# Optimization experiments

Hardware: AMD Instinct MI355X
Metric: run time of the kernel (lower is better)

The kernel has to match this reference:

```python
import jax, jax.numpy as jnp
import numpy as np

UNITS = 300
MDN_MIXES = 8  # Config.mdn_mixes: 3*8=24 MDN params + 1 length = 25-dim feedback
FEAT = 25
GATE_IN = 2 * FEAT  # concat(inputs, prev_output)


def setup_inputs() -> dict:
    key = jax.random.key(0)
    ks = jax.random.split(key, 12)
    B, T = 2048, 512
    x = jax.random.uniform(ks[0], (B, T, FEAT), dtype=jnp.float32)
    s = 0.05
    kernel = jax.random.normal(ks[1], (FEAT, 4 * UNITS), dtype=jnp.float32) * s
    recurrent_kernel = jax.random.normal(ks[2], (UNITS, 4 * UNITS), dtype=jnp.float32) * s
    # unit_forget_bias: zeros except forget-gate slice = ones
    bias = jnp.concatenate([
        jnp.zeros((UNITS,), jnp.float32),
        jnp.ones((UNITS,), jnp.float32),
        jnp.zeros((2 * UNITS,), jnp.float32),
    ])
    # MLPGate: 2-layer MLP combining the two 25-dim distributions -> 24-dim
    mlp_w1 = jax.random.normal(ks[3], (GATE_IN, GATE_IN), dtype=jnp.float32) * s
    mlp_b1 = jnp.zeros((GATE_IN,), jnp.float32)
    mlp_w2 = jax.random.normal(ks[4], (GATE_IN, FEAT - 1), dtype=jnp.float32) * s
    mlp_b2 = jnp.zeros((FEAT - 1,), jnp.float32)
    # MDN heads on h (units -> mdn_mixes each)
    wa = jax.random.normal(ks[5], (UNITS, MDN_MIXES), dtype=jnp.float32) * s
    ba = jnp.zeros((MDN_MIXES,), jnp.float32)
    wm = jax.random.normal(ks[6], (UNITS, MDN_MIXES), dtype=jnp.float32) * s
    bm = jnp.zeros((MDN_MIXES,), jnp.float32)
    ws = jax.random.normal(ks[7], (UNITS, MDN_MIXES), dtype=jnp.float32) * s
    bs = jnp.zeros((MDN_MIXES,), jnp.float32)
    return {
        'x': x, 'kernel': kernel, 'recurrent_kernel': recurrent_kernel, 'bias': bias,
        'mlp_w1': mlp_w1, 'mlp_b1': mlp_b1, 'mlp_w2': mlp_w2, 'mlp_b2': mlp_b2,
        'wa': wa, 'ba': ba, 'wm': wm, 'bm': bm, 'ws': ws, 'bs': bs,
    }


def _hard_sigmoid(z):
    return jnp.clip(0.2 * z + 0.5, 0.0, 1.0)


def _nnelu(z):
    return 1.0 + jax.nn.elu(z)


def reference(x, kernel, recurrent_kernel, bias,
              mlp_w1, mlp_b1, mlp_w2, mlp_b2,
              wa, ba, wm, bm, ws, bs):
    B = x.shape[0]
    dt = x.dtype

    def step(carry, xt):
        h, c, prev = carry  # [B,U], [B,U], [B,25]
        il = xt[:, 24:25]
        pl = prev[:, 24:25]
        combined = il + pl
        denom = jnp.maximum(combined, jnp.asarray(1e-8, dt))  # LengthNormalizer
        inp2 = jnp.concatenate([xt[:, :24], il / denom], axis=1)
        prev2 = jnp.concatenate([prev[:, :24], pl / denom], axis=1)
        # MLP gate combining the two distributions
        g = jax.nn.relu(jnp.concatenate([inp2, prev2], axis=1) @ mlp_w1 + mlp_b1)
        g = g @ mlp_w2 + mlp_b2  # [B,24]
        gate_out = jnp.concatenate([g, combined], axis=1)  # [B,25]
        # LSTM gates (split-kernel math == fused without dropout)
        z = gate_out @ kernel + h @ recurrent_kernel + bias  # [B,4U]
        zi, zf, zc, zo = jnp.split(z, 4, axis=1)
        i = _hard_sigmoid(zi)
        f = _hard_sigmoid(zf)
        o = _hard_sigmoid(zo)
        c_new = f * c + i * jnp.tanh(zc)
        h_new = o * jnp.tanh(c_new)
        # MDN heads
        alpha = jax.nn.softmax(h_new @ wa + ba, axis=-1)
        mu = h_new @ wm + bm
        sigma = _nnelu(h_new @ ws + bs)
        mdn = jnp.concatenate([alpha, mu, sigma, combined], axis=1)  # [B,25]
        return (h_new, c_new, mdn), mdn

    h0 = jnp.zeros((B, UNITS), dt)
    c0 = jnp.zeros((B, UNITS), dt)
    prev0 = jnp.zeros((B, FEAT), dt)
    xt = jnp.swapaxes(x, 0, 1)  # [T,B,25]
    _, ys = jax.lax.scan(step, (h0, c0, prev0), xt)
    return jnp.swapaxes(ys, 0, 1)  # [B,T,25]
```

## Files before the change

kernel.cpp:

```cpp
#include <hip/hip_runtime.h>
#include <math.h>

#define BB 2048
#define TT 512
#define NFEAT 25
#define UNITS 300
#define RPB 16
#define NBLK (BB/RPB)
#define NT 512
#define NKS 11
#define TPW 10
#define AROW 360
#define F8ROW 352
#define GROW 72

#define OFF_B0 0
#define SZ_B0  (8*TPW*512)
#define OFF_M1 (OFF_B0 + SZ_B0)
#define SZ_M1  (4*2*512)
#define OFF_M2 (OFF_M1 + SZ_M1)
#define SZ_M2  (2*2*512)
#define OFF_H  (OFF_M2 + SZ_M2)
#define SZ_H   (2*NKS*512)
#define OFF_F8 (OFF_H + SZ_H)
#define SZ_F8B (8*100*512)
#define SW_SZ  (SZ_M1 + SZ_M2 + SZ_H)
#define SWM1   0
#define SWM2   (SZ_M1)
#define SWH    (SZ_M1 + SZ_M2)

typedef __attribute__((ext_vector_type(4))) float f32x4;
typedef __attribute__((ext_vector_type(8))) short bf16x8;

static __device__ __forceinline__ unsigned short f2bf(float f) {
    union { float f; unsigned u; } x; x.f = f;
    unsigned r = (x.u + 0x7fffu + ((x.u >> 16) & 1u)) >> 16;
    return (unsigned short)r;
}
static __device__ __forceinline__ unsigned char f2f8(float f) {
    return (unsigned char)(__builtin_amdgcn_cvt_pk_fp8_f32(f, 0.f, 0, false) & 0xff);
}
static __device__ __forceinline__ float ftanh(float v) {
    float e = __builtin_amdgcn_exp2f(v * 2.8853900817779268f);
    return 1.f - 2.f * __builtin_amdgcn_rcpf(e + 1.f);
}

static __device__ __forceinline__ int zcol(int c) { return (c & 3) * 300 + (c >> 2); }

__global__ __launch_bounds__(256) void conv_b0(
    const float* __restrict__ wk, unsigned short* __restrict__ dst)
{
    int idx = blockIdx.x * 256 + threadIdx.x;
    if (idx >= SZ_B0) return;
    int j = idx & 7, n = (idx >> 3) & 15, kg = (idx >> 7) & 3, q = idx >> 9;
    int i = q % TPW, w = q / TPW;
    int k = kg * 8 + j, c = (w + 8 * i) * 16 + n;
    float v = (k < 25 && c < 1200) ? wk[k * 1200 + zcol(c)] : 0.f;
    dst[OFF_B0 + idx] = f2bf(v);
}

__global__ __launch_bounds__(256) void conv_b8(
    const float* __restrict__ wr, unsigned char* __restrict__ dst8)
{
    int idx = blockIdx.x * 256 + threadIdx.x;
    if (idx >= SZ_F8B) return;
    int j = idx & 7, n = (idx >> 3) & 15, kg = (idx >> 7) & 3, q = idx >> 9;
    int i = q % TPW, ks1 = (q / TPW) % 10, w = q / 100;
    int k = (ks1 + 1) * 32 + kg * 8 + j, c = (w + 8 * i) * 16 + n;
    float v = (k >= 32 && k < 332 && c < 1200) ? wr[(k - 32) * 1200 + zcol(c)] : 0.f;
    dst8[idx] = f2f8(v);
}

__global__ __launch_bounds__(256) void conv_gen(
    const float* __restrict__ W, unsigned short* __restrict__ dst,
    int K, int N, int nks, int total)
{
    int idx = blockIdx.x * 256 + threadIdx.x;
    if (idx >= total) return;
    int j = idx & 7, n = (idx >> 3) & 15, kg = (idx >> 7) & 3, qq = idx >> 9;
    int ks = qq % nks, nt = qq / nks;
    int k = ks * 32 + kg * 8 + j, col = nt * 16 + n;
    float v = (k < K && col < N) ? W[k * N + col] : 0.f;
    dst[idx] = f2bf(v);
}

__global__ __launch_bounds__(256) void conv_heads(
    const float* __restrict__ wa, const float* __restrict__ wm,
    const float* __restrict__ wsg, unsigned short* __restrict__ dst)
{
    int idx = blockIdx.x * 256 + threadIdx.x;
    if (idx >= SZ_H) return;
    int j = idx & 7, n = (idx >> 3) & 15, kg = (idx >> 7) & 3, qq = idx >> 9;
    int ks = qq % NKS, nt = qq / NKS;
    int k = ks * 32 + kg * 8 + j, col = nt * 16 + n;
    float v = 0.f;
    if (k >= 32 && k < 332 && col < 24) {
        int u = k - 32, h = col >> 3, m = col & 7;
        const float* W = (h == 0) ? wa : (h == 1) ? wm : wsg;
        v = W[u * 8 + m];
    }
    dst[OFF_H + idx] = f2bf(v);
}

#define MFMA   __builtin_amdgcn_mfma_f32_16x16x32_bf16
#define MFMA8  __builtin_amdgcn_mfma_f32_16x16x32_fp8_fp8

__global__ __launch_bounds__(NT, 2)
void dilstm(
    const float* __restrict__ x,
    const unsigned short* __restrict__ wf,
    const float* __restrict__ bz,
    const float* __restrict__ b1v,
    const float* __restrict__ b2v,
    const float* __restrict__ ba,
    const float* __restrict__ bm,
    const float* __restrict__ bs,
    float* __restrict__ out)
{
    __shared__ unsigned short Abf[2][RPB][AROW];
    __shared__ __attribute__((aligned(16))) unsigned char Af8[2][RPB][F8ROW];
    __shared__ unsigned short Gbf[RPB][GROW];
    __shared__ unsigned short G1b[RPB][GROW];
    __shared__ float Sc[RPB][24];
    __shared__ float BzS[1280];
    __shared__ float Zw[8][2][16][20];
    __shared__ unsigned short SW[SW_SZ];

    const int t = threadIdx.x;
    const int lane = t & 63, wv = t >> 6;
    const int arow = lane & 15, akg = lane >> 4;
    const int crow0 = akg * 4;
    const int u_l = lane & 3, rr = lane >> 2;
    const int row0 = blockIdx.x * RPB;

    for (int i = t; i < 2 * RPB * AROW; i += NT) ((unsigned short*)Abf)[i] = 0;
    for (int i = t; i < 2 * RPB * F8ROW; i += NT) ((unsigned char*)Af8)[i] = 0;
    for (int i = t; i < RPB * GROW; i += NT) { ((unsigned short*)Gbf)[i] = 0; ((unsigned short*)G1b)[i] = 0; }
    for (int i = t; i < SW_SZ; i += NT) SW[i] = wf[OFF_M1 + i];
    for (int i = t; i < 1280; i += NT)
        BzS[i] = (i < 1200) ? bz[zcol(i)] : 0.f;

    float m1bias = 0.f, m2bias = 0.f, hbias = 0.f;
    {
        int c1 = wv * 16 + arow;
        if (wv < 4 && c1 < 50) m1bias = b1v[c1];
        if (wv < 2 && c1 < 24) {
            m2bias = b2v[c1];
            hbias = (c1 < 8) ? ba[c1] : (c1 < 16) ? bm[c1 - 8] : bs[c1 - 16];
        }
    }

    float creg[TPW];
    #pragma unroll
    for (int i = 0; i < TPW; ++i) creg[i] = 0.f;

    const unsigned short* bw0 = wf + OFF_B0 + wv * (TPW * 512) + (lane << 3);
    const unsigned char*  bw8 = (const unsigned char*)(wf + OFF_F8) + (size_t)wv * (100 * 512) + (lane << 3);

    const int rA = t / 25, eA = t - (t / 25) * 25;
    float combreg = 0.f, xreg = 0.f;
    if (t < RPB * NFEAT) xreg = x[((size_t)(row0 + rA) * TT) * NFEAT + eA];
    __syncthreads();

    if (t < RPB * NFEAT) {
        if (eA < 24) {
            Gbf[rA][eA] = f2bf(xreg);
        } else {
            float comb = xreg;
            combreg = comb;
            float denom = fmaxf(comb, 1e-8f);
            Gbf[rA][24] = f2bf(xreg / denom);
            Abf[0][rA][24] = f2bf(comb);
        }
    }
    __syncthreads();

    for (int ts = 0; ts < TT; ++ts) {
        const int p = ts & 1;

        if (wv < 4) {
            bf16x8 a0 = *(const bf16x8*)&Gbf[arow][akg * 8];
            bf16x8 a1 = *(const bf16x8*)&Gbf[arow][32 + akg * 8];
            bf16x8 b0 = *(const bf16x8*)&SW[SWM1 + (wv * 2 + 0) * 512 + (lane << 3)];
            bf16x8 b1 = *(const bf16x8*)&SW[SWM1 + (wv * 2 + 1) * 512 + (lane << 3)];
            f32x4 acc1 = {0.f, 0.f, 0.f, 0.f};
            acc1 = MFMA(a0, b0, acc1, 0, 0, 0);
            acc1 = MFMA(a1, b1, acc1, 0, 0, 0);
            int col = wv * 16 + arow;
            if (col < 50) {
                #pragma unroll
                for (int rg = 0; rg < 4; ++rg)
                    G1b[crow0 + rg][col] = f2bf(fmaxf(acc1[rg] + m1bias, 0.f));
            }
        }
        __syncthreads();

        if (wv < 2) {
            bf16x8 a0 = *(const bf16x8*)&G1b[arow][akg * 8];
            bf16x8 a1 = *(const bf16x8*)&G1b[arow][32 + akg * 8];
            bf16x8 b0 = *(const bf16x8*)&SW[SWM2 + (wv * 2 + 0) * 512 + (lane << 3)];
            bf16x8 b1 = *(const bf16x8*)&SW[SWM2 + (wv * 2 + 1) * 512 + (lane << 3)];
            f32x4 acc2 = {0.f, 0.f, 0.f, 0.f};
            acc2 = MFMA(a0, b0, acc2, 0, 0, 0);
            acc2 = MFMA(a1, b1, acc2, 0, 0, 0);
            int col = wv * 16 + arow;
            if (col < 24) {
                #pragma unroll
                for (int rg = 0; rg < 4; ++rg)
                    Abf[p][crow0 + rg][col] = f2bf(acc2[rg] + m2bias);
            }
        }
        __syncthreads();

        {
            if (t < RPB * NFEAT && ts + 1 < TT)
                xreg = x[((size_t)(row0 + rA) * TT + (ts + 1)) * NFEAT + eA];

            f32x4 acc[TPW];
            #pragma unroll
            for (int i = 0; i < TPW; ++i) acc[i] = (f32x4){0.f, 0.f, 0.f, 0.f};

            {
                bf16x8 bb0[TPW];
                #pragma unroll
                for (int i = 0; i < TPW; ++i)
                    bb0[i] = *(const bf16x8*)(bw0 + i * 512);
                bf16x8 aA = *(const bf16x8*)&Abf[p][arow][akg * 8];
                #pragma unroll
                for (int i = 0; i < TPW; ++i)
                    acc[i] = MFMA(aA, bb0[i], acc[i], 0, 0, 0);
            }
            {
                const unsigned char* af8p = &Af8[p][0][0] + arow * F8ROW + akg * 8;
                const unsigned char* bp = bw8;
                long long bbA[TPW], bbB[TPW];
                #pragma unroll
                for (int i = 0; i < TPW; ++i)
                    bbA[i] = *(const long long*)(bp + i * 512);
                #pragma unroll 1
                for (int pr = 0; pr < 5; ++pr) {
                    const int ks = 2 * pr + 1;
                    #pragma unroll
                    for (int i = 0; i < TPW; ++i)
                        bbB[i] = *(const long long*)(bp + 5120 + i * 512);
                    long long a8a = *(const long long*)(af8p + ks * 32);
                    #pragma unroll
                    for (int i = 0; i < TPW; ++i)
                        acc[i] = MFMA8(a8a, bbA[i], acc[i], 0, 0, 0);
                    if (pr < 4) {
                        #pragma unroll
                        for (int i = 0; i < TPW; ++i)
                            bbA[i] = *(const long long*)(bp + 10240 + i * 512);
                    }
                    long long a8b = *(const long long*)(af8p + ks * 32 + 32);
                    #pragma unroll
                    for (int i = 0; i < TPW; ++i)
                        acc[i] = MFMA8(a8b, bbB[i], acc[i], 0, 0, 0);
                    bp += 10240;
                }
            }

            *(f32x4*)&Zw[wv][0][arow][crow0] = acc[0];
            #pragma unroll
            for (int i = 0; i < TPW; ++i) {
                if (i + 1 < TPW)
                    *(f32x4*)&Zw[wv][(i + 1) & 1][arow][crow0] = acc[i + 1];
                f32x4 bz4 = *(const f32x4*)&BzS[(wv + 8 * i) * 16 + 4 * u_l];
                const float* zp = &Zw[wv][i & 1][4 * u_l][rr];
                float zi = zp[0]  + bz4[0];
                float zf = zp[20] + bz4[1];
                float zc = zp[40] + bz4[2];
                float zo = zp[60] + bz4[3];
                if (wv + 8 * i < 75) {
                    float ig = fminf(fmaxf(0.2f * zi + 0.5f, 0.f), 1.f);
                    float fg = fminf(fmaxf(0.2f * zf + 0.5f, 0.f), 1.f);
                    float og = fminf(fmaxf(0.2f * zo + 0.5f, 0.f), 1.f);
                    float cn = fg * creg[i] + ig * ftanh(zc);
                    creg[i] = cn;
                    float hn = og * ftanh(cn);
                    int hc = 32 + (wv + 8 * i) * 4 + u_l;
                    Abf[p ^ 1][rr][hc] = f2bf(hn);
                    Af8[p ^ 1][rr][hc] = f2f8(hn);
                }
            }
        }
        __syncthreads();

        if (wv < 2) {
            f32x4 acc3 = {0.f, 0.f, 0.f, 0.f};
            #pragma unroll
            for (int ks = 1; ks < NKS; ++ks) {
                bf16x8 a = *(const bf16x8*)&Abf[p ^ 1][arow][ks * 32 + akg * 8];
                bf16x8 b = *(const bf16x8*)&SW[SWH + (wv * NKS + ks) * 512 + (lane << 3)];
                acc3 = MFMA(a, b, acc3, 0, 0, 0);
            }
            int col = wv * 16 + arow;
            if (col < 24) {
                #pragma unroll
                for (int rg = 0; rg < 4; ++rg)
                    Sc[crow0 + rg][col] = acc3[rg] + hbias;
            }
        }
        __syncthreads();

        if (t < RPB * NFEAT) {
            float v;
            if (eA < 8) {
                float mx = Sc[rA][0];
                #pragma unroll
                for (int m = 1; m < 8; ++m) mx = fmaxf(mx, Sc[rA][m]);
                float sum = 0.f;
                #pragma unroll
                for (int m = 0; m < 8; ++m)
                    sum += __builtin_amdgcn_exp2f((Sc[rA][m] - mx) * 1.4426950408889634f);
                v = __builtin_amdgcn_exp2f((Sc[rA][eA] - mx) * 1.4426950408889634f) / sum;
            } else if (eA < 16) {
                v = Sc[rA][eA];
            } else if (eA < 24) {
                float s = Sc[rA][eA];
                v = (s > 0.f) ? (1.f + s) : __builtin_amdgcn_exp2f(s * 1.4426950408889634f);
            } else {
                v = combreg;
            }
            out[((size_t)(row0 + rA) * TT + ts) * NFEAT + eA] = v;
            if (eA < 24) {
                Gbf[rA][eA]      = f2bf(xreg);
                Gbf[rA][25 + eA] = f2bf(v);
            } else {
                float comb = xreg + combreg;
                float denom = fmaxf(comb, 1e-8f);
                Gbf[rA][24] = f2bf(xreg / denom);
                Gbf[rA][49] = f2bf(combreg / denom);
                Abf[p ^ 1][rA][24] = f2bf(comb);
                combreg = comb;
            }
        }
        __syncthreads();
    }
}

extern "C" void kernel_launch(void* const* d_in, const int* in_sizes, int n_in,
                              void* d_out, int out_size, void* d_ws, size_t ws_size,
                              hipStream_t stream) {
    const float* x   = (const float*)d_in[0];
    const float* wk  = (const float*)d_in[1];
    const float* wr  = (const float*)d_in[2];
    const float* bz  = (const float*)d_in[3];
    const float* w1  = (const float*)d_in[4];
    const float* b1  = (const float*)d_in[5];
    const float* w2  = (const float*)d_in[6];
    const float* b2  = (const float*)d_in[7];
    const float* wa  = (const float*)d_in[8];
    const float* ba  = (const float*)d_in[9];
    const float* wm  = (const float*)d_in[10];
    const float* bm  = (const float*)d_in[11];
    const float* wsg = (const float*)d_in[12];
    const float* bs  = (const float*)d_in[13];
    float* out = (float*)d_out;
    unsigned short* wf = (unsigned short*)d_ws;
    unsigned char*  wf8 = (unsigned char*)(wf + OFF_F8);

    conv_b0<<<(SZ_B0 + 255) / 256, 256, 0, stream>>>(wk, wf);
    conv_b8<<<(SZ_F8B + 255) / 256, 256, 0, stream>>>(wr, wf8);
    conv_gen<<<(SZ_M1 + 255) / 256, 256, 0, stream>>>(w1, wf + OFF_M1, 50, 50, 2, SZ_M1);
    conv_gen<<<(SZ_M2 + 255) / 256, 256, 0, stream>>>(w2, wf + OFF_M2, 50, 24, 2, SZ_M2);
    conv_heads<<<(SZ_H + 255) / 256, 256, 0, stream>>>(wa, wm, wsg, wf);
    dilstm<<<NBLK, NT, 0, stream>>>(x, wf, bz, b1, b2, ba, bm, bs, out);
}
```

Measured before the change: 3.936 ms.

## Overlap MLP gate with recurrent fp8 matmul, removing one barrier per step

The two-layer MLP gate now runs entirely in wave 0, with biases staged in shared memory. The other waves start the recurrent h·W fp8 MFMA loop at once instead of waiting at two barriers. The input-projection bf16 MFMA is moved after a single barrier so it can read the gate output. This trims per-timestep synchronisation and idle time, but puts the MLP work serially on one wave. Wave 0 relies on intra-wave ordering of its G1b writes before its reads, with no barrier between them.

```diff
diff --git a/kernel.cpp b/kernel.cpp
--- a/kernel.cpp
+++ b/kernel.cpp
@@ -123,6 +123,8 @@
     __shared__ unsigned short G1b[RPB][GROW];
     __shared__ float Sc[RPB][24];
     __shared__ float BzS[1280];
+    __shared__ float B1S[64];
+    __shared__ float B2S[32];
     __shared__ float Zw[8][2][16][20];
     __shared__ unsigned short SW[SW_SZ];
 
@@ -139,15 +141,14 @@
     for (int i = t; i < SW_SZ; i += NT) SW[i] = wf[OFF_M1 + i];
     for (int i = t; i < 1280; i += NT)
         BzS[i] = (i < 1200) ? bz[zcol(i)] : 0.f;
-
-    float m1bias = 0.f, m2bias = 0.f, hbias = 0.f;
+    if (t < 64) B1S[t] = (t < 50) ? b1v[t] : 0.f;
+    else if (t < 96) B2S[t - 64] = (t - 64 < 24) ? b2v[t - 64] : 0.f;
+
+    float hbias = 0.f;
     {
         int c1 = wv * 16 + arow;
-        if (wv < 4 && c1 < 50) m1bias = b1v[c1];
-        if (wv < 2 && c1 < 24) {
-            m2bias = b2v[c1];
+        if (wv < 2 && c1 < 24)
             hbias = (c1 < 8) ? ba[c1] : (c1 < 16) ? bm[c1 - 8] : bs[c1 - 16];
-        }
     }
 
     float creg[TPW];
@@ -178,87 +179,88 @@
     for (int ts = 0; ts < TT; ++ts) {
         const int p = ts & 1;
 
-        if (wv < 4) {
-            bf16x8 a0 = *(const bf16x8*)&Gbf[arow][akg * 8];
-            bf16x8 a1 = *(const bf16x8*)&Gbf[arow][32 + akg * 8];
-            bf16x8 b0 = *(const bf16x8*)&SW[SWM1 + (wv * 2 + 0) * 512 + (lane << 3)];
-            bf16x8 b1 = *(const bf16x8*)&SW[SWM1 + (wv * 2 + 1) * 512 + (lane << 3)];
-            f32x4 acc1 = {0.f, 0.f, 0.f, 0.f};
-            acc1 = MFMA(a0, b0, acc1, 0, 0, 0);
-            acc1 = MFMA(a1, b1, acc1, 0, 0, 0);
-            int col = wv * 16 + arow;
-            if (col < 50) {
-                #pragma unroll
-                for (int rg = 0; rg < 4; ++rg)
-                    G1b[crow0 + rg][col] = f2bf(fmaxf(acc1[rg] + m1bias, 0.f));
-            }
-        }
-        __syncthreads();
-
-        if (wv < 2) {
-            bf16x8 a0 = *(const bf16x8*)&G1b[arow][akg * 8];
-            bf16x8 a1 = *(const bf16x8*)&G1b[arow][32 + akg * 8];
-            bf16x8 b0 = *(const bf16x8*)&SW[SWM2 + (wv * 2 + 0) * 512 + (lane << 3)];
-            bf16x8 b1 = *(const bf16x8*)&SW[SWM2 + (wv * 2 + 1) * 512 + (lane << 3)];
-            f32x4 acc2 = {0.f, 0.f, 0.f, 0.f};
-            acc2 = MFMA(a0, b0, acc2, 0, 0, 0);
-            acc2 = MFMA(a1, b1, acc2, 0, 0, 0);
-            int col = wv * 16 + arow;
-            if (col < 24) {
-                #pragma unroll
-                for (int rg = 0; rg < 4; ++rg)
-                    Abf[p][crow0 + rg][col] = f2bf(acc2[rg] + m2bias);
-            }
-        }
-        __syncthreads();
+        f32x4 acc[TPW];
+        #pragma unroll
+        for (int i = 0; i < TPW; ++i) acc[i] = (f32x4){0.f, 0.f, 0.f, 0.f};
+
+        if (wv == 0) {
+            bf16x8 ga0 = *(const bf16x8*)&Gbf[arow][akg * 8];
+            bf16x8 ga1 = *(const bf16x8*)&Gbf[arow][32 + akg * 8];
+            #pragma unroll
+            for (int ct = 0; ct < 4; ++ct) {
+                bf16x8 b0 = *(const bf16x8*)&SW[SWM1 + (ct * 2 + 0) * 512 + (lane << 3)];
+                bf16x8 b1 = *(const bf16x8*)&SW[SWM1 + (ct * 2 + 1) * 512 + (lane << 3)];
+                f32x4 a1c = {0.f, 0.f, 0.f, 0.f};
+                a1c = MFMA(ga0, b0, a1c, 0, 0, 0);
+                a1c = MFMA(ga1, b1, a1c, 0, 0, 0);
+                int col = ct * 16 + arow;
+                if (col < 50) {
+                    #pragma unroll
+                    for (int rg = 0; rg < 4; ++rg)
+                        G1b[crow0 + rg][col] = f2bf(fmaxf(a1c[rg] + B1S[col], 0.f));
+                }
+            }
+            bf16x8 ha0 = *(const bf16x8*)&G1b[arow][akg * 8];
+            bf16x8 ha1 = *(const bf16x8*)&G1b[arow][32 + akg * 8];
+            #pragma unroll
+            for (int ct = 0; ct < 2; ++ct) {
+                bf16x8 b0 = *(const bf16x8*)&SW[SWM2 + (ct * 2 + 0) * 512 + (lane << 3)];
+                bf16x8 b1 = *(const bf16x8*)&SW[SWM2 + (ct * 2 + 1) * 512 + (lane << 3)];
+                f32x4 a2c = {0.f, 0.f, 0.f, 0.f};
+                a2c = MFMA(ha0, b0, a2c, 0, 0, 0);
+                a2c = MFMA(ha1, b1, a2c, 0, 0, 0);
+                int col = ct * 16 + arow;
+                if (col < 24) {
+                    #pragma unroll
+                    for (int rg = 0; rg < 4; ++rg)
+                        Abf[p][crow0 + rg][col] = f2bf(a2c[rg] + B2S[col]);
+                }
+            }
+        }
+
+        if (t < RPB * NFEAT && ts + 1 < TT)
+            xreg = x[((size_t)(row0 + rA) * TT + (ts + 1)) * NFEAT + eA];
 
         {
-            if (t < RPB * NFEAT && ts + 1 < TT)
-                xreg = x[((size_t)(row0 + rA) * TT + (ts + 1)) * NFEAT + eA];
-
-            f32x4 acc[TPW];
-            #pragma unroll
-            for (int i = 0; i < TPW; ++i) acc[i] = (f32x4){0.f, 0.f, 0.f, 0.f};
-
-            {
-                bf16x8 bb0[TPW];
+            const unsigned char* af8p = &Af8[p][0][0] + arow * F8ROW + akg * 8;
+            const unsigned char* bp = bw8;
+            long long bbA[TPW], bbB[TPW];
+            #pragma unroll
+            for (int i = 0; i < TPW; ++i)
+                bbA[i] = *(const long long*)(bp + i * 512);
+            #pragma unroll 1
+            for (int pr = 0; pr < 5; ++pr) {
+                const int ks = 2 * pr + 1;
                 #pragma unroll
                 for (int i = 0; i < TPW; ++i)
-                    bb0[i] = *(const bf16x8*)(bw0 + i * 512);
-                bf16x8 aA = *(const bf16x8*)&Abf[p][arow][akg * 8];
+                    bbB[i] = *(const long long*)(bp + 5120 + i * 512);
+                long long a8a = *(const long long*)(af8p + ks * 32);
                 #pragma unroll
                 for (int i = 0; i < TPW; ++i)
-                    acc[i] = MFMA(aA, bb0[i], acc[i], 0, 0, 0);
-            }
-            {
-                const unsigned char* af8p = &Af8[p][0][0] + arow * F8ROW + akg * 8;
-                const unsigned char* bp = bw8;
-                long long bbA[TPW], bbB[TPW];
-                #pragma unroll
-                for (int i = 0; i < TPW; ++i)
-                    bbA[i] = *(const long long*)(bp + i * 512);
-                #pragma unroll 1
-                for (int pr = 0; pr < 5; ++pr) {
-                    const int ks = 2 * pr + 1;
+                    acc[i] = MFMA8(a8a, bbA[i], acc[i], 0, 0, 0);
+                if (pr < 4) {
                     #pragma unroll
                     for (int i = 0; i < TPW; ++i)
-                        bbB[i] = *(const long long*)(bp + 5120 + i * 512);
-                    long long a8a = *(const long long*)(af8p + ks * 32);
-                    #pragma unroll
-                    for (int i = 0; i < TPW; ++i)
-                        acc[i] = MFMA8(a8a, bbA[i], acc[i], 0, 0, 0);
-                    if (pr < 4) {
-                        #pragma unroll
-                        for (int i = 0; i < TPW; ++i)
-                            bbA[i] = *(const long long*)(bp + 10240 + i * 512);
-                    }
-                    long long a8b = *(const long long*)(af8p + ks * 32 + 32);
-                    #pragma unroll
-                    for (int i = 0; i < TPW; ++i)
-                        acc[i] = MFMA8(a8b, bbB[i], acc[i], 0, 0, 0);
-                    bp += 10240;
+                        bbA[i] = *(const long long*)(bp + 10240 + i * 512);
                 }
-            }
+                long long a8b = *(const long long*)(af8p + ks * 32 + 32);
+                #pragma unroll
+                for (int i = 0; i < TPW; ++i)
+                    acc[i] = MFMA8(a8b, bbB[i], acc[i], 0, 0, 0);
+                bp += 10240;
+            }
+        }
+        __syncthreads();
+
+        {
+            bf16x8 bb0[TPW];
+            #pragma unroll
+            for (int i = 0; i < TPW; ++i)
+                bb0[i] = *(const bf16x8*)(bw0 + i * 512);
+            bf16x8 aA = *(const bf16x8*)&Abf[p][arow][akg * 8];
+            #pragma unroll
+            for (int i = 0; i < TPW; ++i)
+                acc[i] = MFMA(aA, bb0[i], acc[i], 0, 0, 0);
 
             *(f32x4*)&Zw[wv][0][arow][crow0] = acc[0];
             #pragma unroll
```

Result: slower. 4.139 ms (+5.2%).
